# Performance work log

Hardware: AMD Instinct MI355X
Metric: run time of the kernel (lower is better)

The kernel has to match this reference:

```python
import jax, jax.numpy as jnp
import numpy as np

B, N, M, C, H = 8, 2048, 1024, 512, 8
D = C // H  # per-head dim = 64


def setup_inputs() -> dict:
    key = jax.random.key(0)
    ks = jax.random.split(key, 4)
    x = jax.random.normal(ks[0], (B, N, C), dtype=jnp.float32)
    global_tokens = jax.random.normal(ks[1], (B, M, C), dtype=jnp.float32)
    Wq = jax.random.normal(ks[2], (C, C), dtype=jnp.float32) * 0.02
    bq = jnp.zeros((C,), dtype=jnp.float32)
    Wkv = jax.random.normal(ks[3], (C, 2 * C), dtype=jnp.float32) * 0.02
    bkv = jnp.zeros((2 * C,), dtype=jnp.float32)
    return {"x": x, "global_tokens": global_tokens, "Wq": Wq, "bq": bq,
            "Wkv": Wkv, "bkv": bkv}


def reference(x, global_tokens, Wq, bq, Wkv, bkv):
    # q from x, k/v from global_tokens (LinearProjection with query=True)
    q = (x @ Wq + bq).reshape(B, N, H, D).transpose(0, 2, 1, 3)        # [B,H,N,D]
    kv = (global_tokens @ Wkv + bkv).reshape(B, M, 2, H, D)
    k = kv[:, :, 0].transpose(0, 2, 1, 3)                              # [B,H,M,D]
    v = kv[:, :, 1].transpose(0, 2, 1, 3)                              # [B,H,M,D]
    # NOTE: original module applies no 1/sqrt(D) scaling in forward
    attn = jnp.einsum('bhnd,bhmd->bhnm', q, k)                         # [B,H,N,M]
    attn = jax.nn.softmax(attn, axis=-1)
    out = jnp.einsum('bhnm,bhmd->bhnd', attn, v)                       # [B,H,N,D]
    return out.transpose(0, 2, 1, 3).reshape(B, N, C)
```

## Files before the change

### kernel.cpp

```cpp
#include <hip/hip_runtime.h>
#include <hip/hip_bf16.h>


typedef __bf16 bf16_t;
typedef __bf16 bf16x8 __attribute__((ext_vector_type(8)));
typedef __bf16 bf16x4 __attribute__((ext_vector_type(4)));
typedef float floatx16 __attribute__((ext_vector_type(16)));
typedef unsigned int uintx4 __attribute__((ext_vector_type(4)));
typedef unsigned int uintx2 __attribute__((ext_vector_type(2)));

#define KDIM 512
#define QSCALE 1.44269504088896f

__device__ __forceinline__ unsigned pack2(float a, float b) {
  unsigned short ua = __builtin_bit_cast(unsigned short, (bf16_t)a);
  unsigned short ub = __builtin_bit_cast(unsigned short, (bf16_t)b);
  return (unsigned)ua | ((unsigned)ub << 16);
}

__device__ __forceinline__ float fexp2(float x) {
#if __has_builtin(__builtin_amdgcn_exp2f)
  return __builtin_amdgcn_exp2f(x);
#else
  return __exp2f(x);
#endif
}

__device__ __forceinline__ bf16x8 cvt8(const float4 a, const float4 b) {
  bf16x8 r;
  r[0] = (bf16_t)a.x; r[1] = (bf16_t)a.y; r[2] = (bf16_t)a.z; r[3] = (bf16_t)a.w;
  r[4] = (bf16_t)b.x; r[5] = (bf16_t)b.y; r[6] = (bf16_t)b.z; r[7] = (bf16_t)b.w;
  return r;
}

__device__ __forceinline__ void gl_lds16(const bf16_t* g, bf16_t* l) {
#if __has_builtin(__builtin_amdgcn_global_load_lds)
  __builtin_amdgcn_global_load_lds(
      (const __attribute__((address_space(1))) unsigned int*)(g),
      (__attribute__((address_space(3))) unsigned int*)(l), 16, 0, 0);
#else
  *(bf16x8*)l = *(const bf16x8*)g;
#endif
}

__global__ __launch_bounds__(256) void transpose_cvt_kernel(
    const float* __restrict__ Wq, const float* __restrict__ Wkv,
    bf16_t* __restrict__ Wqt, bf16_t* __restrict__ Wkvt) {
  __shared__ float tile[64][65];
  const int blk = blockIdx.x;
  const float* in; bf16_t* out; int N, bx, by;
  if (blk < 64) { in = Wq; out = Wqt; N = 512; bx = blk & 7; by = blk >> 3; }
  else { int t2 = blk - 64; in = Wkv; out = Wkvt; N = 1024; bx = t2 & 15; by = t2 >> 4; }
  const int t = threadIdx.x;
  const int c0 = bx * 64, k0 = by * 64;
#pragma unroll
  for (int i = 0; i < 16; ++i) {
    int idx = t + i * 256;
    int kk = idx >> 6, cc = idx & 63;
    tile[kk][cc] = in[(size_t)(k0 + kk) * N + (c0 + cc)];
  }
  __syncthreads();
#pragma unroll
  for (int j = 0; j < 2; ++j) {
    int unit = t + j * 256;
    int cc = unit >> 3, ks = (unit & 7) * 8;
    int c = c0 + cc, k = k0 + ks;
    bf16x8 v;
#pragma unroll
    for (int i = 0; i < 8; ++i) v[i] = (bf16_t)tile[ks + i][cc];
    *(bf16x8*)(&out[(size_t)((c >> 7) * 16 + (k >> 5)) * 4096 + (c & 127) * 32 + (k & 31)]) = v;
  }
}

__global__ __launch_bounds__(256) void proj_gemm_kernel(
    const float* __restrict__ x, const float* __restrict__ gt,
    const bf16_t* __restrict__ Wqt, const bf16_t* __restrict__ Wkvt,
    const float* __restrict__ bq, const float* __restrict__ bkv,
    bf16_t* __restrict__ Qf, bf16_t* __restrict__ Kf, bf16_t* __restrict__ Vf) {
  __shared__ bf16_t lA[128 * 40];
  __shared__ bf16_t lW[4096];
  const int blk = blockIdx.x;
  int mode, bx, by;
  const float* A; const bf16_t* Wt; const float* bias;
  if (blk < 512) { mode = 0; bx = blk & 3; by = blk >> 2; A = x; Wt = Wqt; bias = bq; }
  else { int tt = blk - 512; mode = 1; bx = tt & 7; by = tt >> 3; A = gt; Wt = Wkvt; bias = bkv; }

  const int tid = threadIdx.x;
  const int wave = tid >> 6, L = tid & 63;
  const int l5 = L & 31, hf = L >> 5;
  const int wr = wave >> 1, wc = wave & 1;
  const int rb = by * 128, cb = bx * 128;

  floatx16 acc[2][2] = {};

  const int arow = tid >> 1, akq = (tid & 1) * 16;
  const float* Ap = A + (size_t)(rb + arow) * KDIM + akq;
  bf16_t* lAw = &lA[arow * 40 + akq];
  const bf16_t* Wbase = Wt + (size_t)bx * 16 * 4096;

  float4 f0 = *(const float4*)(Ap);
  float4 f1 = *(const float4*)(Ap + 4);
  float4 f2 = *(const float4*)(Ap + 8);
  float4 f3 = *(const float4*)(Ap + 12);

  for (int kt = 0; kt < 16; ++kt) {
    __syncthreads();
#pragma unroll
    for (int j = 0; j < 2; ++j) {
      const int s = wave * 2 + j;
      gl_lds16(Wbase + (size_t)kt * 4096 + s * 512 + L * 8, &lW[s * 512 + L * 8]);
    }
    *(bf16x8*)(lAw) = cvt8(f0, f1);
    *(bf16x8*)(lAw + 8) = cvt8(f2, f3);
    __syncthreads();
    if (kt < 15) {
      Ap += 32;
      f0 = *(const float4*)(Ap);
      f1 = *(const float4*)(Ap + 4);
      f2 = *(const float4*)(Ap + 8);
      f3 = *(const float4*)(Ap + 12);
    }
    bf16x8 af[2][2], wf[2][2];
#pragma unroll
    for (int rs = 0; rs < 2; ++rs)
#pragma unroll
      for (int kh = 0; kh < 2; ++kh)
        af[rs][kh] = *(const bf16x8*)(&lA[(wr * 64 + rs * 32 + l5) * 40 + kh * 16 + hf * 8]);
#pragma unroll
    for (int cs = 0; cs < 2; ++cs)
#pragma unroll
      for (int kh = 0; kh < 2; ++kh)
        wf[cs][kh] = *(const bf16x8*)(&lW[(wc * 64 + cs * 32 + l5) * 32 + kh * 16 + hf * 8]);
#pragma unroll
    for (int rs = 0; rs < 2; ++rs)
#pragma unroll
      for (int cs = 0; cs < 2; ++cs)
#pragma unroll
        for (int kh = 0; kh < 2; ++kh)
          acc[rs][cs] = __builtin_amdgcn_mfma_f32_32x32x16_bf16(
              af[rs][kh], wf[cs][kh], acc[rs][cs], 0, 0, 0);
  }

#pragma unroll
  for (int rs = 0; rs < 2; ++rs)
#pragma unroll
    for (int cs = 0; cs < 2; ++cs) {
      const int col = cb + wc * 64 + cs * 32 + l5;
      const float bv = bias[col];
      const int grb = rb + wr * 64 + rs * 32;
      if (mode == 0) {
        const int hh = col >> 6, d = col & 63;
        const int dof = (d >> 3) * 256 + (d & 7);
#pragma unroll
        for (int r = 0; r < 16; ++r) {
          int gr = grb + (r & 3) + 8 * (r >> 2) + 4 * hf;
          int b = gr >> 11, n = gr & 2047;
          Qf[(size_t)(b * 8 + hh) * 131072 + (n >> 5) * 2048 + dof + (n & 31) * 8] =
              (bf16_t)((acc[rs][cs][r] + bv) * QSCALE);
        }
      } else if (col < 512) {
        const int hh = col >> 6, d = col & 63;
        const int dof = (d >> 3) * 256 + (d & 7);
#pragma unroll
        for (int r = 0; r < 16; ++r) {
          int gr = grb + (r & 3) + 8 * (r >> 2) + 4 * hf;
          int b = gr >> 10, m = gr & 1023;
          Kf[(size_t)(b * 8 + hh) * 65536 + (m >> 5) * 2048 + dof + (m & 31) * 8] =
              (bf16_t)(acc[rs][cs][r] + bv);
        }
      } else {
        const int cc = col - 512;
        const int hh = cc >> 6, d = cc & 63;
        const int dof = (d >> 5) * 1024 + (d & 31) * 8;
#pragma unroll
        for (int rq = 0; rq < 4; ++rq) {
          int gr = grb + 8 * rq + 4 * hf;
          int b = gr >> 10, m = gr & 1023;
          bf16x4 pk;
          pk[0] = (bf16_t)(acc[rs][cs][rq * 4 + 0] + bv);
          pk[1] = (bf16_t)(acc[rs][cs][rq * 4 + 1] + bv);
          pk[2] = (bf16_t)(acc[rs][cs][rq * 4 + 2] + bv);
          pk[3] = (bf16_t)(acc[rs][cs][rq * 4 + 3] + bv);
          *(bf16x4*)(&Vf[(size_t)(b * 8 + hh) * 65536 + (m >> 5) * 2048 + dof +
                         ((m >> 4) & 1) * 512 + ((m >> 3) & 1) * 256 + (m & 7)]) = pk;
        }
      }
    }
}

__global__ __launch_bounds__(256, 4) void flash_attn_kernel(
    const bf16_t* __restrict__ Qf, const bf16_t* __restrict__ Kf,
    const bf16_t* __restrict__ Vf, float* __restrict__ out) {
  __shared__ bf16_t kv[2][4096];
  __shared__ float lo[4][32 * 36];
  const int tid = threadIdx.x;
  const int wave = tid >> 6, L = tid & 63;
  const int l5 = L & 31, hf = L >> 5;
  const int bh = blockIdx.y;
  const int b = bh >> 3, hh = bh & 7;
  const int nb = blockIdx.x * 128 + wave * 32;

  const bf16_t* Qp = Qf + (size_t)bh * 131072 + (nb >> 5) * 2048 + L * 8;
  const bf16_t* Kb = Kf + (size_t)bh * 65536;
  const bf16_t* Vb = Vf + (size_t)bh * 65536;

  bf16x8 qf[4];
#pragma unroll
  for (int kc = 0; kc < 4; ++kc) qf[kc] = *(const bf16x8*)(Qp + kc * 512);

  floatx16 o0 = {}, o1 = {};
  float lpa = 0.f, lpb = 0.f;

  auto dma = [&](int buf, int sb) {
#pragma unroll
    for (int j = 0; j < 2; ++j) {
      const int s = wave * 2 + j;
      const bf16_t* g = (s < 4) ? (Kb + (size_t)sb * 2048 + s * 512 + L * 8)
                                : (Vb + (size_t)sb * 2048 + (s - 4) * 512 + L * 8);
      bf16_t* l = &kv[buf][(s < 4 ? s * 512 : 2048 + (s - 4) * 512) + L * 8];
      gl_lds16(g, l);
    }
  };

  dma(0, 0);
  __syncthreads();

  for (int sb = 0; sb < 32; ++sb) {
    const int cur = sb & 1;
    if (sb < 31) dma(cur ^ 1, sb + 1);
    const bf16_t* kb = &kv[cur][0];
    const bf16_t* vb = &kv[cur][2048];
    bf16x8 kf[4];
#pragma unroll
    for (int kc = 0; kc < 4; ++kc) kf[kc] = *(const bf16x8*)(kb + kc * 512 + L * 8);
    floatx16 sa = {};
#pragma unroll
    for (int kc = 0; kc < 4; ++kc)
      sa = __builtin_amdgcn_mfma_f32_32x32x16_bf16(kf[kc], qf[kc], sa, 0, 0, 0);
    bf16x8 vf[4];
#pragma unroll
    for (int j = 0; j < 4; ++j) vf[j] = *(const bf16x8*)(vb + j * 512 + L * 8);
    unsigned w[8];
#pragma unroll
    for (int i = 0; i < 8; ++i) {
      float pa = fexp2(sa[2 * i]), pb = fexp2(sa[2 * i + 1]);
      lpa += pa; lpb += pb;
      w[i] = pack2(pa, pb);
    }
    uintx4 fw0, fw1;
#if __has_builtin(__builtin_amdgcn_permlane32_swap)
    {
      uintx2 r0 = __builtin_amdgcn_permlane32_swap(w[0], w[2], false, false);
      uintx2 r1 = __builtin_amdgcn_permlane32_swap(w[1], w[3], false, false);
      uintx2 r2 = __builtin_amdgcn_permlane32_swap(w[4], w[6], false, false);
      uintx2 r3 = __builtin_amdgcn_permlane32_swap(w[5], w[7], false, false);
      fw0.x = r0[0]; fw0.z = r0[1];
      fw0.y = r1[0]; fw0.w = r1[1];
      fw1.x = r2[0]; fw1.z = r2[1];
      fw1.y = r3[0]; fw1.w = r3[1];
    }
#else
    {
      unsigned sw[8];
#pragma unroll
      for (int i = 0; i < 8; ++i) sw[i] = __shfl_xor(w[i], 32);
      fw0.x = hf ? sw[2] : w[0]; fw0.y = hf ? sw[3] : w[1];
      fw0.z = hf ? w[2] : sw[0]; fw0.w = hf ? w[3] : sw[1];
      fw1.x = hf ? sw[6] : w[4]; fw1.y = hf ? sw[7] : w[5];
      fw1.z = hf ? w[6] : sw[4]; fw1.w = hf ? w[7] : sw[5];
    }
#endif
    bf16x8 pf0 = __builtin_bit_cast(bf16x8, fw0);
    bf16x8 pf1 = __builtin_bit_cast(bf16x8, fw1);
    o0 = __builtin_amdgcn_mfma_f32_32x32x16_bf16(vf[0], pf0, o0, 0, 0, 0);
    o0 = __builtin_amdgcn_mfma_f32_32x32x16_bf16(vf[1], pf1, o0, 0, 0, 0);
    o1 = __builtin_amdgcn_mfma_f32_32x32x16_bf16(vf[2], pf0, o1, 0, 0, 0);
    o1 = __builtin_amdgcn_mfma_f32_32x32x16_bf16(vf[3], pf1, o1, 0, 0, 0);
    __syncthreads();
  }

  float lp = lpa + lpb;
  lp += __shfl_xor(lp, 32);
  const float inv = 1.0f / lp;

  float* lob = lo[wave];
  const size_t orow = (size_t)b * 2048 + nb;
#pragma unroll
  for (int pass = 0; pass < 2; ++pass) {
    const floatx16& oo = pass ? o1 : o0;
#pragma unroll
    for (int i = 0; i < 8; ++i) {
      const int d = 2 * (i & 1) + 8 * (i >> 1) + 4 * hf;
      float2 a;
      a.x = oo[2 * i] * inv; a.y = oo[2 * i + 1] * inv;
      *(float2*)(&lob[l5 * 36 + d]) = a;
    }
#pragma unroll
    for (int j = 0; j < 4; ++j) {
      int chunk = j * 64 + L;
      int n = chunk >> 3, c = chunk & 7;
      float4 v = *(const float4*)(&lob[n * 36 + c * 4]);
      *(float4*)(&out[(orow + n) * 512 + hh * 64 + pass * 32 + c * 4]) = v;
    }
  }
}

extern "C" void kernel_launch(void* const* d_in, const int* in_sizes, int n_in,
                              void* d_out, int out_size, void* d_ws, size_t ws_size,
                              hipStream_t stream) {
  (void)in_sizes; (void)n_in; (void)out_size; (void)ws_size;
  const float* x   = (const float*)d_in[0];
  const float* gt  = (const float*)d_in[1];
  const float* Wq  = (const float*)d_in[2];
  const float* bq  = (const float*)d_in[3];
  const float* Wkv = (const float*)d_in[4];
  const float* bkv = (const float*)d_in[5];
  float* out = (float*)d_out;

  bf16_t* Wqt  = (bf16_t*)d_ws;
  bf16_t* Wkvt = Wqt + (size_t)512 * 512;
  bf16_t* Qf   = Wkvt + (size_t)1024 * 512;
  bf16_t* Kf   = Qf + (size_t)64 * 2048 * 64;
  bf16_t* Vf   = Kf + (size_t)64 * 1024 * 64;

  transpose_cvt_kernel<<<192, 256, 0, stream>>>(Wq, Wkv, Wqt, Wkvt);
  proj_gemm_kernel<<<1024, 256, 0, stream>>>(x, gt, Wqt, Wkvt, bq, bkv, Qf, Kf, Vf);
  flash_attn_kernel<<<dim3(16, 64), 256, 0, stream>>>(Qf, Kf, Vf, out);
}
```

Baseline: 184.3 us.

## Double KV tile per barrier, compute softmax denominator via MFMA, reuse LDS for output

Each pipeline stage now loads two 32-key K/V sub-tiles, halving the number of __syncthreads per block. The row-sum of exp values is computed with an MFMA against an all-ones operand instead of per-lane VALU adds plus a cross-half shuffle. The separate output staging buffer is dropped by aliasing it onto the KV LDS buffer. Together these trade extra MFMA work and larger LDS per stage for fewer barriers and less VALU work; the row sum is now built from bf16-rounded probabilities.

```diff
diff --git a/kernel.cpp b/kernel.cpp
--- a/kernel.cpp
+++ b/kernel.cpp
@@ -191,8 +191,7 @@
 __global__ __launch_bounds__(256, 4) void flash_attn_kernel(
     const bf16_t* __restrict__ Qf, const bf16_t* __restrict__ Kf,
     const bf16_t* __restrict__ Vf, float* __restrict__ out) {
-  __shared__ bf16_t kv[2][4096];
-  __shared__ float lo[4][32 * 36];
+  __shared__ bf16_t kv[2][2][4096];
   const int tid = threadIdx.x;
   const int wave = tid >> 6, L = tid & 63;
   const int l5 = L & 31, hf = L >> 5;
@@ -201,23 +200,27 @@
   const int nb = blockIdx.x * 128 + wave * 32;
 
   const bf16_t* Qp = Qf + (size_t)bh * 131072 + (nb >> 5) * 2048 + L * 8;
-  const bf16_t* Kb = Kf + (size_t)bh * 65536;
-  const bf16_t* Vb = Vf + (size_t)bh * 65536;
+  const bf16_t* Kb = Kf + (size_t)bh * 65536 + L * 8;
+  const bf16_t* Vb = Vf + (size_t)bh * 65536 + L * 8;
 
   bf16x8 qf[4];
 #pragma unroll
   for (int kc = 0; kc < 4; ++kc) qf[kc] = *(const bf16x8*)(Qp + kc * 512);
 
-  floatx16 o0 = {}, o1 = {};
-  float lpa = 0.f, lpb = 0.f;
-
-  auto dma = [&](int buf, int sb) {
-#pragma unroll
-    for (int j = 0; j < 2; ++j) {
-      const int s = wave * 2 + j;
-      const bf16_t* g = (s < 4) ? (Kb + (size_t)sb * 2048 + s * 512 + L * 8)
-                                : (Vb + (size_t)sb * 2048 + (s - 4) * 512 + L * 8);
-      bf16_t* l = &kv[buf][(s < 4 ? s * 512 : 2048 + (s - 4) * 512) + L * 8];
+  bf16x8 ones;
+#pragma unroll
+  for (int i = 0; i < 8; ++i) ones[i] = (bf16_t)1.0f;
+
+  floatx16 o0 = {}, o1 = {}, lacc = {};
+
+  auto dma = [&](int buf, int ep2) {
+#pragma unroll
+    for (int j = 0; j < 4; ++j) {
+      const int s = wave * 4 + j;
+      const int sub = s >> 3, q = s & 7;
+      const bf16_t* g = (q < 4) ? (Kb + (size_t)(ep2 * 2 + sub) * 2048 + q * 512)
+                                : (Vb + (size_t)(ep2 * 2 + sub) * 2048 + (q - 4) * 512);
+      bf16_t* l = &kv[buf][sub][(q < 4 ? q * 512 : 2048 + (q - 4) * 512) + L * 8];
       gl_lds16(g, l);
     }
   };
@@ -225,65 +228,67 @@
   dma(0, 0);
   __syncthreads();
 
-  for (int sb = 0; sb < 32; ++sb) {
-    const int cur = sb & 1;
-    if (sb < 31) dma(cur ^ 1, sb + 1);
-    const bf16_t* kb = &kv[cur][0];
-    const bf16_t* vb = &kv[cur][2048];
-    bf16x8 kf[4];
-#pragma unroll
-    for (int kc = 0; kc < 4; ++kc) kf[kc] = *(const bf16x8*)(kb + kc * 512 + L * 8);
-    floatx16 sa = {};
-#pragma unroll
-    for (int kc = 0; kc < 4; ++kc)
-      sa = __builtin_amdgcn_mfma_f32_32x32x16_bf16(kf[kc], qf[kc], sa, 0, 0, 0);
-    bf16x8 vf[4];
-#pragma unroll
-    for (int j = 0; j < 4; ++j) vf[j] = *(const bf16x8*)(vb + j * 512 + L * 8);
-    unsigned w[8];
-#pragma unroll
-    for (int i = 0; i < 8; ++i) {
-      float pa = fexp2(sa[2 * i]), pb = fexp2(sa[2 * i + 1]);
-      lpa += pa; lpb += pb;
-      w[i] = pack2(pa, pb);
-    }
-    uintx4 fw0, fw1;
+  for (int ep = 0; ep < 16; ++ep) {
+    const int cur = ep & 1;
+    if (ep < 15) dma(cur ^ 1, ep + 1);
+#pragma unroll
+    for (int sub = 0; sub < 2; ++sub) {
+      const bf16_t* kb = &kv[cur][sub][L * 8];
+      const bf16_t* vb = &kv[cur][sub][2048 + L * 8];
+      bf16x8 kf4[4];
+#pragma unroll
+      for (int kc = 0; kc < 4; ++kc) kf4[kc] = *(const bf16x8*)(kb + kc * 512);
+      floatx16 sa = {};
+#pragma unroll
+      for (int kc = 0; kc < 4; ++kc)
+        sa = __builtin_amdgcn_mfma_f32_32x32x16_bf16(kf4[kc], qf[kc], sa, 0, 0, 0);
+      bf16x8 vf4[4];
+#pragma unroll
+      for (int j = 0; j < 4; ++j) vf4[j] = *(const bf16x8*)(vb + j * 512);
+      unsigned w[8];
+#pragma unroll
+      for (int i = 0; i < 8; ++i) {
+        float pa = fexp2(sa[2 * i]), pb = fexp2(sa[2 * i + 1]);
+        w[i] = pack2(pa, pb);
+      }
+      uintx4 fw0, fw1;
 #if __has_builtin(__builtin_amdgcn_permlane32_swap)
-    {
-      uintx2 r0 = __builtin_amdgcn_permlane32_swap(w[0], w[2], false, false);
-      uintx2 r1 = __builtin_amdgcn_permlane32_swap(w[1], w[3], false, false);
-      uintx2 r2 = __builtin_amdgcn_permlane32_swap(w[4], w[6], false, false);
-      uintx2 r3 = __builtin_amdgcn_permlane32_swap(w[5], w[7], false, false);
-      fw0.x = r0[0]; fw0.z = r0[1];
-      fw0.y = r1[0]; fw0.w = r1[1];
-      fw1.x = r2[0]; fw1.z = r2[1];
-      fw1.y = r3[0]; fw1.w = r3[1];
-    }
+      {
+        uintx2 r0 = __builtin_amdgcn_permlane32_swap(w[0], w[2], false, false);
+        uintx2 r1 = __builtin_amdgcn_permlane32_swap(w[1], w[3], false, false);
+        uintx2 r2 = __builtin_amdgcn_permlane32_swap(w[4], w[6], false, false);
+        uintx2 r3 = __builtin_amdgcn_permlane32_swap(w[5], w[7], false, false);
+        fw0.x = r0[0]; fw0.z = r0[1];
+        fw0.y = r1[0]; fw0.w = r1[1];
+        fw1.x = r2[0]; fw1.z = r2[1];
+        fw1.y = r3[0]; fw1.w = r3[1];
+      }
 #else
-    {
-      unsigned sw[8];
-#pragma unroll
-      for (int i = 0; i < 8; ++i) sw[i] = __shfl_xor(w[i], 32);
-      fw0.x = hf ? sw[2] : w[0]; fw0.y = hf ? sw[3] : w[1];
-      fw0.z = hf ? w[2] : sw[0]; fw0.w = hf ? w[3] : sw[1];
-      fw1.x = hf ? sw[6] : w[4]; fw1.y = hf ? sw[7] : w[5];
-      fw1.z = hf ? w[6] : sw[4]; fw1.w = hf ? w[7] : sw[5];
-    }
+      {
+        unsigned sw[8];
+#pragma unroll
+        for (int i = 0; i < 8; ++i) sw[i] = __shfl_xor(w[i], 32);
+        fw0.x = hf ? sw[2] : w[0]; fw0.y = hf ? sw[3] : w[1];
+        fw0.z = hf ? w[2] : sw[0]; fw0.w = hf ? w[3] : sw[1];
+        fw1.x = hf ? sw[6] : w[4]; fw1.y = hf ? sw[7] : w[5];
+        fw1.z = hf ? w[6] : sw[4]; fw1.w = hf ? w[7] : sw[5];
+      }
 #endif
-    bf16x8 pf0 = __builtin_bit_cast(bf16x8, fw0);
-    bf16x8 pf1 = __builtin_bit_cast(bf16x8, fw1);
-    o0 = __builtin_amdgcn_mfma_f32_32x32x16_bf16(vf[0], pf0, o0, 0, 0, 0);
-    o0 = __builtin_amdgcn_mfma_f32_32x32x16_bf16(vf[1], pf1, o0, 0, 0, 0);
-    o1 = __builtin_amdgcn_mfma_f32_32x32x16_bf16(vf[2], pf0, o1, 0, 0, 0);
-    o1 = __builtin_amdgcn_mfma_f32_32x32x16_bf16(vf[3], pf1, o1, 0, 0, 0);
+      bf16x8 pf0 = __builtin_bit_cast(bf16x8, fw0);
+      bf16x8 pf1 = __builtin_bit_cast(bf16x8, fw1);
+      lacc = __builtin_amdgcn_mfma_f32_32x32x16_bf16(ones, pf0, lacc, 0, 0, 0);
+      lacc = __builtin_amdgcn_mfma_f32_32x32x16_bf16(ones, pf1, lacc, 0, 0, 0);
+      o0 = __builtin_amdgcn_mfma_f32_32x32x16_bf16(vf4[0], pf0, o0, 0, 0, 0);
+      o0 = __builtin_amdgcn_mfma_f32_32x32x16_bf16(vf4[1], pf1, o0, 0, 0, 0);
+      o1 = __builtin_amdgcn_mfma_f32_32x32x16_bf16(vf4[2], pf0, o1, 0, 0, 0);
+      o1 = __builtin_amdgcn_mfma_f32_32x32x16_bf16(vf4[3], pf1, o1, 0, 0, 0);
+    }
     __syncthreads();
   }
 
-  float lp = lpa + lpb;
-  lp += __shfl_xor(lp, 32);
-  const float inv = 1.0f / lp;
-
-  float* lob = lo[wave];
+  const float inv = 1.0f / lacc[0];
+
+  float* lob = (float*)(&kv[0][0][0]) + wave * (32 * 36);
   const size_t orow = (size_t)b * 2048 + nb;
 #pragma unroll
   for (int pass = 0; pass < 2; ++pass) {
```

Measured after the change: 182.9 us. No clear change (-0.7%).
